# Kernel tuning notes

Hardware: AMD Instinct MI355X
Metric: run time of the kernel (lower is better)

The kernel has to match this reference:

```python
import jax, jax.numpy as jnp
import numpy as np

B, N, C = 8, 196, 512
NC, H = 10, 8
HD = C // H
SCALE = HD ** -0.5


def setup_inputs() -> dict:
    key = jax.random.key(0)
    ks = jax.random.split(key, 8)
    s = 1.0 / np.sqrt(C)
    return {
        "x": jax.random.normal(ks[0], (B, N, C), jnp.float32),
        "anchors": jax.random.normal(ks[1], (NC, N, C), jnp.float32),
        "weights": jax.random.uniform(ks[2], (B, H, NC), jnp.float32),
        "Wqk": jax.random.normal(ks[3], (C, C), jnp.float32) * s,
        "Wqk2": jax.random.normal(ks[4], (C, C), jnp.float32) * s,
        "Wv": jax.random.normal(ks[5], (C, C), jnp.float32) * s,
        "Wproj": jax.random.normal(ks[6], (C, C), jnp.float32) * s,
        "bproj": jax.random.normal(ks[7], (C,), jnp.float32) * 0.01,
    }


def _heads(t):
    # (..., N, C) -> (..., H, N, HD)
    shp = t.shape[:-2]
    return t.reshape(shp + (t.shape[-2], H, HD)).swapaxes(-3, -2)


def reference(x, anchors, weights, Wqk, Wqk2, Wv, Wproj, bproj):
    v = _heads(x @ Wv)                      # (B, H, N, HD)
    q = _heads(x @ Wqk)[:, None]            # (B, 1, H, N, HD)
    k = _heads(anchors @ Wqk)[None]         # (1, NC, H, N, HD)
    q2 = _heads(x @ Wqk2)[:, None]          # (B, 1, H, N, HD)
    k2 = _heads(anchors @ Wqk2)[None]       # (1, NC, H, N, HD)

    # ReLU-clipped double attention, both (B, NC, H, N, N)
    left_attn = jnp.maximum(-(q @ k.swapaxes(-2, -1)) * SCALE, 0.0)
    right_attn = jnp.maximum((k2 @ q2.swapaxes(-2, -1)) * SCALE, 0.0)

    attn = left_attn @ right_attn           # (B, NC, H, N, N)
    # per-head class-weighted combine: (B,H,NC) x (B,NC,H,N,N) -> (B,H,N,N)
    tmp = jnp.einsum('bhc,bchnm->bhnm', weights, attn)
    out = tmp @ v                           # (B, H, N, HD)
    # NOTE: original torch code reshapes (B,H,N,HD)->(B,N,C) WITHOUT a
    # transpose back; we replicate that exact flatten order.
    out = out.reshape(B, N, C)
    out = out @ Wproj + bproj
    return (out, left_attn)
```

## Files before the change

kernel.cpp:

```cpp
#include <hip/hip_runtime.h>

#define OFF_XB     0u
#define OFF_AB     1605632u
#define OFF_WQKT   3612672u
#define OFF_WQK2T  4136960u
#define OFF_WVT    4661248u
#define OFF_WPROJT 5185536u
#define OFF_XQ     5709824u
#define OFF_XQ2    7315456u
#define OFF_XV     8921088u
#define OFF_AQ     10526720u
#define OFF_AQ2    12533760u
#define OFF_RVT    14540800u
#define OFF_OUT1   35512320u
#define OFF_P      37117952u

typedef __attribute__((ext_vector_type(8))) short bf16x8;
typedef __attribute__((ext_vector_type(4))) float f32x4;
#define MFMA(a, b, c) __builtin_amdgcn_mfma_f32_16x16x32_bf16((a), (b), (c), 0, 0, 0)

__device__ __forceinline__ unsigned short f2bf(float x) {
  unsigned u = __builtin_bit_cast(unsigned, x);
  u += 0x7fffu + ((u >> 16) & 1u);
  return (unsigned short)(u >> 16);
}
__device__ __forceinline__ float bf2f(unsigned short s) {
  return __builtin_bit_cast(float, ((unsigned)s) << 16);
}

__device__ __forceinline__ void gl_lds16(const void* g, void* l) {
  __builtin_amdgcn_global_load_lds(
      (const __attribute__((address_space(1))) unsigned int*)g,
      (__attribute__((address_space(3))) unsigned int*)l, 16, 0, 0);
}

__device__ __forceinline__ void stage64(const unsigned short* g0, int stride,
                                        unsigned short (*T)[72], int tid, int nrows) {
  int wv = tid >> 6;
  char* base = (char*)&T[0][0];
#pragma unroll
  for (int i = 0; i < 2; i++) {
    int k = i * 256 + tid;
    int r = k / 9, c = k - r * 9;
    if (r < nrows)
      gl_lds16(g0 + (size_t)r * stride + (c << 3), base + (((i << 2) + wv) << 10));
  }
  if (tid < 64) {
    int k = 512 + tid;
    int r = k / 9, c = k - r * 9;
    if (r < nrows)
      gl_lds16(g0 + (size_t)r * stride + (c << 3), base + 8192);
  }
}

__device__ __forceinline__ void load_bf16_tile(unsigned short T[64][72], const unsigned short* __restrict__ g,
                                               int row0, int nrows, int col0, int tid) {
  int r = tid >> 2;
  int c0 = (tid & 3) << 4;
  uint4 a = make_uint4(0, 0, 0, 0), b = make_uint4(0, 0, 0, 0);
  if (r < nrows) {
    const unsigned short* p = g + (size_t)(row0 + r) * 512 + col0 + c0;
    a = *(const uint4*)p;
    b = *(const uint4*)(p + 8);
  }
  *(uint4*)&T[r][c0] = a;
  *(uint4*)&T[r][c0 + 8] = b;
}

__device__ __forceinline__ void load_bf16_tile_T(unsigned short T[64][72], const unsigned short* __restrict__ g,
                                                 int row0, int nrows, int col0, int tid) {
#pragma unroll
  for (int rep = 0; rep < 2; rep++) {
    int j = (tid >> 3) + (rep << 5);
    int d0 = (tid & 7) << 3;
    uint4 a = make_uint4(0, 0, 0, 0);
    if (j < nrows) a = *(const uint4*)(g + (size_t)(row0 + j) * 512 + col0 + d0);
    unsigned short s[8];
    *(uint4*)s = a;
#pragma unroll
    for (int u = 0; u < 8; u++) T[d0 + u][j] = s[u];
  }
}

__global__ __launch_bounds__(256) void pre_kernel(const float* __restrict__ x, const float* __restrict__ anchors,
                                                  const float* __restrict__ Wqk, const float* __restrict__ Wqk2,
                                                  const float* __restrict__ Wv, const float* __restrict__ Wproj,
                                                  char* __restrict__ ws) {
  int tid = threadIdx.x;
  if (blockIdx.x < 1764) {
    int base = blockIdx.x * 1024 + (tid << 2);
    float4 f = (base < 802816) ? *(const float4*)(x + base)
                               : *(const float4*)(anchors + (base - 802816));
    unsigned short s[4] = {f2bf(f.x), f2bf(f.y), f2bf(f.z), f2bf(f.w)};
    *(uint2*)((unsigned short*)(ws + OFF_XB) + base) = *(uint2*)s;
    return;
  }
  __shared__ unsigned short Ls[64][72];
  int idx = blockIdx.x - 1764;
  int wsel = idx >> 6, t = idx & 63;
  int k0 = (t >> 3) << 6, n0 = (t & 7) << 6;
  const float* W;
  unsigned short* WT;
  switch (wsel) {
    case 0:  W = Wqk;   WT = (unsigned short*)(ws + OFF_WQKT);   break;
    case 1:  W = Wqk2;  WT = (unsigned short*)(ws + OFF_WQK2T);  break;
    case 2:  W = Wv;    WT = (unsigned short*)(ws + OFF_WVT);    break;
    default: W = Wproj; WT = (unsigned short*)(ws + OFF_WPROJT); break;
  }
  {
    int r = tid >> 2, seg = (tid & 3) << 4;
    const float* p = W + (size_t)(k0 + r) * 512 + n0 + seg;
    float4 f0 = *(const float4*)p, f1 = *(const float4*)(p + 4);
    float4 f2 = *(const float4*)(p + 8), f3 = *(const float4*)(p + 12);
    unsigned short s[16] = {f2bf(f0.x), f2bf(f0.y), f2bf(f0.z), f2bf(f0.w),
                            f2bf(f1.x), f2bf(f1.y), f2bf(f1.z), f2bf(f1.w),
                            f2bf(f2.x), f2bf(f2.y), f2bf(f2.z), f2bf(f2.w),
                            f2bf(f3.x), f2bf(f3.y), f2bf(f3.z), f2bf(f3.w)};
    *(uint4*)&Ls[r][seg] = *(uint4*)s;
    *(uint4*)&Ls[r][seg + 8] = *(uint4*)(s + 8);
  }
  __syncthreads();
  {
    int r = tid >> 2, seg = (tid & 3) << 4;
    unsigned short s[16];
#pragma unroll
    for (int u = 0; u < 16; u++) s[u] = Ls[seg + u][r];
    unsigned short* dst = WT + (size_t)(n0 + r) * 512 + k0 + seg;
    *(uint4*)dst = *(uint4*)s;
    *(uint4*)(dst + 8) = *(uint4*)(s + 8);
  }
}

template <bool STORE_BF16>
__device__ __forceinline__ void gemm_bf16_body(const unsigned short* __restrict__ A,
                                               const unsigned short* __restrict__ WT,
                                               const float* __restrict__ bias, void* __restrict__ outp,
                                               int M, int row_blk, int col_blk) {
  __shared__ unsigned short As[64][72];
  __shared__ unsigned short Ws[64][72];
  int row0 = row_blk << 6;
  if (row0 >= M) return;
  int col0 = col_blk << 6;
  int tid = threadIdx.x;
  int w = tid >> 6, lm = tid & 15, lq = (tid >> 4) & 3;
  f32x4 acc[4] = {};
  for (int k0 = 0; k0 < 512; k0 += 64) {
    __syncthreads();
    stage64(A + (size_t)row0 * 512 + k0, 512, As, tid, 64);
    stage64(WT + (size_t)col0 * 512 + k0, 512, Ws, tid, 64);
    __syncthreads();
#pragma unroll
    for (int kk = 0; kk < 2; kk++) {
      bf16x8 bf = *(const bf16x8*)&Ws[(w << 4) + lm][(kk << 5) + (lq << 3)];
#pragma unroll
      for (int mi = 0; mi < 4; mi++) {
        bf16x8 af = *(const bf16x8*)&As[(mi << 4) + lm][(kk << 5) + (lq << 3)];
        acc[mi] = MFMA(af, bf, acc[mi]);
      }
    }
  }
  int ncol = col0 + (w << 4) + lm;
  float bv = bias ? bias[ncol] : 0.f;
#pragma unroll
  for (int mi = 0; mi < 4; mi++)
#pragma unroll
    for (int r2 = 0; r2 < 4; r2++) {
      int row = row0 + (mi << 4) + (lq << 2) + r2;
      if (row < M) {
        if (STORE_BF16)
          ((unsigned short*)outp)[(size_t)row * 512 + ncol] = f2bf(acc[mi][r2]);
        else
          ((float*)outp)[(size_t)row * 512 + ncol] = acc[mi][r2] + bv;
      }
    }
}

__global__ __launch_bounds__(256) void proj5(char* __restrict__ ws) {
  const unsigned short* xb = (const unsigned short*)(ws + OFF_XB);
  const unsigned short* ab = (const unsigned short*)(ws + OFF_AB);
  const unsigned short* A; const unsigned short* WT; unsigned short* O; int M;
  switch (blockIdx.z) {
    case 0:  A = xb; WT = (unsigned short*)(ws + OFF_WQKT);  O = (unsigned short*)(ws + OFF_XQ);  M = 1568; break;
    case 1:  A = xb; WT = (unsigned short*)(ws + OFF_WQK2T); O = (unsigned short*)(ws + OFF_XQ2); M = 1568; break;
    case 2:  A = xb; WT = (unsigned short*)(ws + OFF_WVT);   O = (unsigned short*)(ws + OFF_XV);  M = 1568; break;
    case 3:  A = ab; WT = (unsigned short*)(ws + OFF_WQKT);  O = (unsigned short*)(ws + OFF_AQ);  M = 1960; break;
    default: A = ab; WT = (unsigned short*)(ws + OFF_WQK2T); O = (unsigned short*)(ws + OFF_AQ2); M = 1960; break;
  }
  gemm_bf16_body<true>(A, WT, nullptr, O, M, blockIdx.x, blockIdx.y);
}

__global__ __launch_bounds__(256) void final_gemm(const unsigned short* __restrict__ out1,
                                                  const unsigned short* __restrict__ WT,
                                                  const float* __restrict__ bias, float* __restrict__ out) {
  gemm_bf16_body<false>(out1, WT, bias, out, 1568, blockIdx.x, blockIdx.y);
}

__global__ __launch_bounds__(256) void rv_mfma(char* __restrict__ ws) {
  const unsigned short* xq2 = (const unsigned short*)(ws + OFF_XQ2);
  const unsigned short* aq2 = (const unsigned short*)(ws + OFF_AQ2);
  const unsigned short* xv  = (const unsigned short*)(ws + OFF_XV);
  unsigned short* rvt       = (unsigned short*)(ws + OFF_RVT);
  __shared__ unsigned short Ks[64][72];
  __shared__ unsigned short Qs[64][72];
  __shared__ unsigned short Vt[64][72];
  __shared__ unsigned short Ss[64][72];
  int i0 = blockIdx.x << 6;
  int bch = blockIdx.y;
  int h = bch & 7, bc = bch >> 3;
  int c = bc % 10, b = bc / 10;
  int tid = threadIdx.x;
  int w = tid >> 6, lm = tid & 15, lq = (tid >> 4) & 3;
  int ni = min(64, 196 - i0);

  load_bf16_tile(Ks, aq2, c * 196 + i0, ni, h << 6, tid);
  __syncthreads();
  bf16x8 kf[4][2];
#pragma unroll
  for (int mi = 0; mi < 4; mi++)
#pragma unroll
    for (int kk = 0; kk < 2; kk++)
      kf[mi][kk] = *(const bf16x8*)&Ks[(mi << 4) + lm][(kk << 5) + (lq << 3)];

  f32x4 acc[4] = {};
  for (int jt = 0; jt < 4; jt++) {
    int j0 = jt << 6;
    int nj = min(64, 196 - j0);
    __syncthreads();
    stage64(xq2 + (size_t)(b * 196 + j0) * 512 + (h << 6), 512, Qs, tid, 64);
    load_bf16_tile_T(Vt, xv, b * 196 + j0, nj, h << 6, tid);
    __syncthreads();
    f32x4 s[4] = {};
#pragma unroll
    for (int kk = 0; kk < 2; kk++) {
      bf16x8 bf = *(const bf16x8*)&Qs[(w << 4) + lm][(kk << 5) + (lq << 3)];
#pragma unroll
      for (int mi = 0; mi < 4; mi++) s[mi] = MFMA(kf[mi][kk], bf, s[mi]);
    }
#pragma unroll
    for (int mi = 0; mi < 4; mi++)
#pragma unroll
      for (int r = 0; r < 4; r++)
        Ss[(mi << 4) + (lq << 2) + r][(w << 4) + lm] = f2bf(fmaxf(0.125f * s[mi][r], 0.f));
    __syncthreads();
#pragma unroll
    for (int kk = 0; kk < 2; kk++) {
      bf16x8 bf = *(const bf16x8*)&Vt[(w << 4) + lm][(kk << 5) + (lq << 3)];
#pragma unroll
      for (int mi = 0; mi < 4; mi++) {
        bf16x8 af = *(const bf16x8*)&Ss[(mi << 4) + lm][(kk << 5) + (lq << 3)];
        acc[mi] = MFMA(af, bf, acc[mi]);
      }
    }
  }
  __syncthreads();
#pragma unroll
  for (int mi = 0; mi < 4; mi++)
#pragma unroll
    for (int r = 0; r < 4; r++)
      Ss[(w << 4) + lm][(mi << 4) + (lq << 2) + r] = f2bf(acc[mi][r]);
  __syncthreads();
  {
    int dd = tid >> 2, seg = (tid & 3) << 4;
    unsigned short* dst = rvt + ((size_t)(bch * 4 + blockIdx.x) * 64 + dd) * 64 + seg;
    *(uint4*)dst = *(uint4*)&Ss[dd][seg];
    *(uint4*)(dst + 8) = *(uint4*)&Ss[dd][seg + 8];
  }
}

__global__ __launch_bounds__(256) void attn_mfma(char* __restrict__ ws, float* __restrict__ left,
                                                 unsigned short* __restrict__ P) {
  const unsigned short* xq  = (const unsigned short*)(ws + OFF_XQ);
  const unsigned short* aq  = (const unsigned short*)(ws + OFF_AQ);
  const unsigned short* rvt = (const unsigned short*)(ws + OFF_RVT);
  __shared__ unsigned short Qs[64][72];
  __shared__ unsigned short Ks[64][72];
  __shared__ unsigned short Rt[64][72];
  __shared__ unsigned short Ss[64][72];
  int i0 = blockIdx.x << 6;
  int bh = blockIdx.y;
  int c = blockIdx.z;
  int b = bh >> 3, h = bh & 7;
  int bch = (b * 10 + c) * 8 + h;
  int tid = threadIdx.x;
  int w = tid >> 6, lm = tid & 15, lq = (tid >> 4) & 3;

  stage64(xq + (size_t)(b * 196 + i0) * 512 + (h << 6), 512, Qs, tid, 64);
  bf16x8 qf[4][2];
  f32x4 acc[4] = {};
  size_t lbase = (size_t)bch * (196 * 196);
#pragma unroll
  for (int t = 0; t < 4; t++) {
    int jt = (t == 0) ? 3 : t - 1;
    int j0 = jt << 6;
    int nj = (jt == 3) ? 4 : 64;
    __syncthreads();
    if (t == 0) {
      uint4 z = make_uint4(0, 0, 0, 0);
      for (int k = tid; k < 540; k += 256)
        *(uint4*)((char*)&Ks[0][0] + 576 + k * 16) = z;
    }
    stage64(aq + (size_t)(c * 196 + j0) * 512 + (h << 6), 512, Ks, tid, nj);
    stage64(rvt + (size_t)(bch * 4 + jt) * 4096, 64, Rt, tid, 64);
    __syncthreads();
    if (t == 0) {
#pragma unroll
      for (int mi = 0; mi < 4; mi++)
#pragma unroll
        for (int kk = 0; kk < 2; kk++)
          qf[mi][kk] = *(const bf16x8*)&Qs[(mi << 4) + lm][(kk << 5) + (lq << 3)];
    }
    f32x4 s[4] = {};
#pragma unroll
    for (int kk = 0; kk < 2; kk++) {
      bf16x8 bf = *(const bf16x8*)&Ks[(w << 4) + lm][(kk << 5) + (lq << 3)];
#pragma unroll
      for (int mi = 0; mi < 4; mi++) s[mi] = MFMA(qf[mi][kk], bf, s[mi]);
    }
#pragma unroll
    for (int mi = 0; mi < 4; mi++)
#pragma unroll
      for (int r = 0; r < 4; r++) {
        float v = fmaxf(-0.125f * s[mi][r], 0.f);
        int il = (mi << 4) + (lq << 2) + r;
        int jl = (w << 4) + lm;
        Ss[il][jl] = f2bf(v);
        if (i0 + il < 196 && j0 + jl < 196)
          left[lbase + (size_t)(i0 + il) * 196 + (j0 + jl)] = v;
      }
    __syncthreads();
#pragma unroll
    for (int kk = 0; kk < 2; kk++) {
      bf16x8 bf = *(const bf16x8*)&Rt[(w << 4) + lm][(kk << 5) + (lq << 3)];
#pragma unroll
      for (int mi = 0; mi < 4; mi++) {
        bf16x8 af = *(const bf16x8*)&Ss[(mi << 4) + lm][(kk << 5) + (lq << 3)];
        acc[mi] = MFMA(af, bf, acc[mi]);
      }
    }
  }
  __syncthreads();
#pragma unroll
  for (int mi = 0; mi < 4; mi++)
#pragma unroll
    for (int r = 0; r < 4; r++)
      Ss[(mi << 4) + (lq << 2) + r][(w << 4) + lm] = f2bf(acc[mi][r]);
  __syncthreads();
  {
    int row = tid >> 2, seg = (tid & 3) << 4;
    if (i0 + row < 196) {
      unsigned short* dst = P + ((size_t)(bh * 10 + c) * 196 + i0 + row) * 64 + seg;
      *(uint4*)dst = *(uint4*)&Ss[row][seg];
      *(uint4*)(dst + 8) = *(uint4*)&Ss[row][seg + 8];
    }
  }
}

__global__ __launch_bounds__(256) void reduce_out1(const unsigned short* __restrict__ P,
                                                   const float* __restrict__ weights,
                                                   unsigned short* __restrict__ out1) {
  int t = blockIdx.x * 256 + threadIdx.x;
  int base = t << 2;
  int bh = base / 12544;
  int rem = base - bh * 12544;
  const float* wrow = weights + bh * 10;
  float a0 = 0.f, a1 = 0.f, a2 = 0.f, a3 = 0.f;
#pragma unroll
  for (int c = 0; c < 10; c++) {
    float wc = wrow[c];
    const unsigned short* p = P + ((size_t)(bh * 10 + c)) * 12544 + rem;
    ushort4 u = *(const ushort4*)p;
    a0 = fmaf(wc, bf2f(u.x), a0);
    a1 = fmaf(wc, bf2f(u.y), a1);
    a2 = fmaf(wc, bf2f(u.z), a2);
    a3 = fmaf(wc, bf2f(u.w), a3);
  }
  unsigned short s[4] = {f2bf(a0), f2bf(a1), f2bf(a2), f2bf(a3)};
  *(uint2*)&out1[base] = *(uint2*)s;
}

extern "C" void kernel_launch(void* const* d_in, const int* in_sizes, int n_in,
                              void* d_out, int out_size, void* d_ws, size_t ws_size,
                              hipStream_t stream) {
  (void)in_sizes; (void)n_in; (void)out_size; (void)ws_size;
  const float* x       = (const float*)d_in[0];
  const float* anchors = (const float*)d_in[1];
  const float* weights = (const float*)d_in[2];
  const float* Wqk     = (const float*)d_in[3];
  const float* Wqk2    = (const float*)d_in[4];
  const float* Wv      = (const float*)d_in[5];
  const float* Wproj   = (const float*)d_in[6];
  const float* bproj   = (const float*)d_in[7];
  char* ws = (char*)d_ws;
  float* out  = (float*)d_out;
  float* left = out + 802816;

  dim3 blk(256);
  pre_kernel<<<dim3(2020), blk, 0, stream>>>(x, anchors, Wqk, Wqk2, Wv, Wproj, ws);
  proj5<<<dim3(31, 8, 5), blk, 0, stream>>>(ws);
  rv_mfma<<<dim3(4, 640), blk, 0, stream>>>(ws);
  attn_mfma<<<dim3(4, 64, 10), blk, 0, stream>>>(ws, left, (unsigned short*)(ws + OFF_P));
  reduce_out1<<<dim3(784), blk, 0, stream>>>((const unsigned short*)(ws + OFF_P), weights,
                                             (unsigned short*)(ws + OFF_OUT1));
  final_gemm<<<dim3(25, 8), blk, 0, stream>>>((const unsigned short*)(ws + OFF_OUT1),
                                              (const unsigned short*)(ws + OFF_WPROJT), bproj, out);
}
```

Before: 231.2 us.

## Fuse right-attention-times-V and left-attention kernels into one per-(b,c,h) block

Merges the rv_mfma and attn_mfma kernels into one kernel with one block per (batch, class, head). The right_attn@V product is kept in registers (rf) and is no longer written to and re-read from the workspace, and one kernel launch is removed. In exchange the grid shrinks from 2560 blocks per kernel to 640, each doing four times more serial work, which may reduce parallelism and latency hiding on a GPU with many CUs.

```diff
diff --git a/kernel.cpp b/kernel.cpp
--- a/kernel.cpp
+++ b/kernel.cpp
@@ -195,162 +195,150 @@
   gemm_bf16_body<false>(out1, WT, bias, out, 1568, blockIdx.x, blockIdx.y);
 }
 
-__global__ __launch_bounds__(256) void rv_mfma(char* __restrict__ ws) {
+__global__ __launch_bounds__(256) void rv_attn(char* __restrict__ ws, float* __restrict__ left,
+                                               unsigned short* __restrict__ P) {
   const unsigned short* xq2 = (const unsigned short*)(ws + OFF_XQ2);
   const unsigned short* aq2 = (const unsigned short*)(ws + OFF_AQ2);
   const unsigned short* xv  = (const unsigned short*)(ws + OFF_XV);
-  unsigned short* rvt       = (unsigned short*)(ws + OFF_RVT);
+  const unsigned short* xq  = (const unsigned short*)(ws + OFF_XQ);
+  const unsigned short* aq  = (const unsigned short*)(ws + OFF_AQ);
   __shared__ unsigned short Ks[64][72];
   __shared__ unsigned short Qs[64][72];
   __shared__ unsigned short Vt[64][72];
   __shared__ unsigned short Ss[64][72];
-  int i0 = blockIdx.x << 6;
-  int bch = blockIdx.y;
+  int bch = blockIdx.x;
   int h = bch & 7, bc = bch >> 3;
   int c = bc % 10, b = bc / 10;
+  int bh = (b << 3) + h;
   int tid = threadIdx.x;
   int w = tid >> 6, lm = tid & 15, lq = (tid >> 4) & 3;
-  int ni = min(64, 196 - i0);
-
-  load_bf16_tile(Ks, aq2, c * 196 + i0, ni, h << 6, tid);
-  __syncthreads();
-  bf16x8 kf[4][2];
-#pragma unroll
-  for (int mi = 0; mi < 4; mi++)
+
+  bf16x8 rf[4][2];
+
+#pragma unroll
+  for (int it = 0; it < 4; it++) {
+    int i0 = it << 6;
+    int ni = (it == 3) ? 4 : 64;
+    load_bf16_tile(Ks, aq2, c * 196 + i0, ni, h << 6, tid);
+    __syncthreads();
+    bf16x8 kf[4][2];
+#pragma unroll
+    for (int mi = 0; mi < 4; mi++)
+#pragma unroll
+      for (int kk = 0; kk < 2; kk++)
+        kf[mi][kk] = *(const bf16x8*)&Ks[(mi << 4) + lm][(kk << 5) + (lq << 3)];
+
+    f32x4 acc[4] = {};
+    for (int jt = 0; jt < 4; jt++) {
+      int j0 = jt << 6;
+      int nj = min(64, 196 - j0);
+      __syncthreads();
+      stage64(xq2 + (size_t)(b * 196 + j0) * 512 + (h << 6), 512, Qs, tid, 64);
+      load_bf16_tile_T(Vt, xv, b * 196 + j0, nj, h << 6, tid);
+      __syncthreads();
+      f32x4 s[4] = {};
+#pragma unroll
+      for (int kk = 0; kk < 2; kk++) {
+        bf16x8 bf = *(const bf16x8*)&Qs[(w << 4) + lm][(kk << 5) + (lq << 3)];
+#pragma unroll
+        for (int mi = 0; mi < 4; mi++) s[mi] = MFMA(kf[mi][kk], bf, s[mi]);
+      }
+#pragma unroll
+      for (int mi = 0; mi < 4; mi++)
+#pragma unroll
+        for (int r = 0; r < 4; r++)
+          Ss[(mi << 4) + (lq << 2) + r][(w << 4) + lm] = f2bf(fmaxf(0.125f * s[mi][r], 0.f));
+      __syncthreads();
+#pragma unroll
+      for (int kk = 0; kk < 2; kk++) {
+        bf16x8 bf = *(const bf16x8*)&Vt[(w << 4) + lm][(kk << 5) + (lq << 3)];
+#pragma unroll
+        for (int mi = 0; mi < 4; mi++) {
+          bf16x8 af = *(const bf16x8*)&Ss[(mi << 4) + lm][(kk << 5) + (lq << 3)];
+          acc[mi] = MFMA(af, bf, acc[mi]);
+        }
+      }
+    }
+    __syncthreads();
+#pragma unroll
+    for (int mi = 0; mi < 4; mi++)
+#pragma unroll
+      for (int r = 0; r < 4; r++)
+        Ss[(w << 4) + lm][(mi << 4) + (lq << 2) + r] = f2bf(acc[mi][r]);
+    __syncthreads();
 #pragma unroll
     for (int kk = 0; kk < 2; kk++)
-      kf[mi][kk] = *(const bf16x8*)&Ks[(mi << 4) + lm][(kk << 5) + (lq << 3)];
-
-  f32x4 acc[4] = {};
-  for (int jt = 0; jt < 4; jt++) {
-    int j0 = jt << 6;
-    int nj = min(64, 196 - j0);
-    __syncthreads();
-    stage64(xq2 + (size_t)(b * 196 + j0) * 512 + (h << 6), 512, Qs, tid, 64);
-    load_bf16_tile_T(Vt, xv, b * 196 + j0, nj, h << 6, tid);
-    __syncthreads();
-    f32x4 s[4] = {};
-#pragma unroll
-    for (int kk = 0; kk < 2; kk++) {
-      bf16x8 bf = *(const bf16x8*)&Qs[(w << 4) + lm][(kk << 5) + (lq << 3)];
-#pragma unroll
-      for (int mi = 0; mi < 4; mi++) s[mi] = MFMA(kf[mi][kk], bf, s[mi]);
-    }
+      rf[it][kk] = *(const bf16x8*)&Ss[(w << 4) + lm][(kk << 5) + (lq << 3)];
+  }
+
+  size_t lbase = (size_t)bch * (196 * 196);
+  for (int it = 0; it < 4; it++) {
+    int i0 = it << 6;
+    stage64(xq + (size_t)(b * 196 + i0) * 512 + (h << 6), 512, Qs, tid, 64);
+    bf16x8 qf[4][2];
+    f32x4 acc[4] = {};
+#pragma unroll
+    for (int t = 0; t < 4; t++) {
+      int jt = (t == 0) ? 3 : t - 1;
+      int j0 = jt << 6;
+      int nj = (jt == 3) ? 4 : 64;
+      __syncthreads();
+      if (t == 0) {
+        uint4 z = make_uint4(0, 0, 0, 0);
+        for (int k = tid; k < 540; k += 256)
+          *(uint4*)((char*)&Ks[0][0] + 576 + k * 16) = z;
+      }
+      stage64(aq + (size_t)(c * 196 + j0) * 512 + (h << 6), 512, Ks, tid, nj);
+      __syncthreads();
+      if (t == 0) {
+#pragma unroll
+        for (int mi = 0; mi < 4; mi++)
+#pragma unroll
+          for (int kk = 0; kk < 2; kk++)
+            qf[mi][kk] = *(const bf16x8*)&Qs[(mi << 4) + lm][(kk << 5) + (lq << 3)];
+      }
+      f32x4 s[4] = {};
+#pragma unroll
+      for (int kk = 0; kk < 2; kk++) {
+        bf16x8 bf = *(const bf16x8*)&Ks[(w << 4) + lm][(kk << 5) + (lq << 3)];
+#pragma unroll
+        for (int mi = 0; mi < 4; mi++) s[mi] = MFMA(qf[mi][kk], bf, s[mi]);
+      }
+#pragma unroll
+      for (int mi = 0; mi < 4; mi++)
+#pragma unroll
+        for (int r = 0; r < 4; r++) {
+          float v = fmaxf(-0.125f * s[mi][r], 0.f);
+          int il = (mi << 4) + (lq << 2) + r;
+          int jl = (w << 4) + lm;
+          Ss[il][jl] = f2bf(v);
+          if (i0 + il < 196 && j0 + jl < 196)
+            left[lbase + (size_t)(i0 + il) * 196 + (j0 + jl)] = v;
+        }
+      __syncthreads();
+#pragma unroll
+      for (int kk = 0; kk < 2; kk++) {
+#pragma unroll
+        for (int mi = 0; mi < 4; mi++) {
+          bf16x8 af = *(const bf16x8*)&Ss[(mi << 4) + lm][(kk << 5) + (lq << 3)];
+          acc[mi] = MFMA(af, rf[jt][kk], acc[mi]);
+        }
+      }
+    }
+    __syncthreads();
 #pragma unroll
     for (int mi = 0; mi < 4; mi++)
 #pragma unroll
       for (int r = 0; r < 4; r++)
-        Ss[(mi << 4) + (lq << 2) + r][(w << 4) + lm] = f2bf(fmaxf(0.125f * s[mi][r], 0.f));
-    __syncthreads();
-#pragma unroll
-    for (int kk = 0; kk < 2; kk++) {
-      bf16x8 bf = *(const bf16x8*)&Vt[(w << 4) + lm][(kk << 5) + (lq << 3)];
-#pragma unroll
-      for (int mi = 0; mi < 4; mi++) {
-        bf16x8 af = *(const bf16x8*)&Ss[(mi << 4) + lm][(kk << 5) + (lq << 3)];
-        acc[mi] = MFMA(af, bf, acc[mi]);
-      }
-    }
-  }
-  __syncthreads();
-#pragma unroll
-  for (int mi = 0; mi < 4; mi++)
-#pragma unroll
-    for (int r = 0; r < 4; r++)
-      Ss[(w << 4) + lm][(mi << 4) + (lq << 2) + r] = f2bf(acc[mi][r]);
-  __syncthreads();
-  {
-    int dd = tid >> 2, seg = (tid & 3) << 4;
-    unsigned short* dst = rvt + ((size_t)(bch * 4 + blockIdx.x) * 64 + dd) * 64 + seg;
-    *(uint4*)dst = *(uint4*)&Ss[dd][seg];
-    *(uint4*)(dst + 8) = *(uint4*)&Ss[dd][seg + 8];
-  }
-}
-
-__global__ __launch_bounds__(256) void attn_mfma(char* __restrict__ ws, float* __restrict__ left,
-                                                 unsigned short* __restrict__ P) {
-  const unsigned short* xq  = (const unsigned short*)(ws + OFF_XQ);
-  const unsigned short* aq  = (const unsigned short*)(ws + OFF_AQ);
-  const unsigned short* rvt = (const unsigned short*)(ws + OFF_RVT);
-  __shared__ unsigned short Qs[64][72];
-  __shared__ unsigned short Ks[64][72];
-  __shared__ unsigned short Rt[64][72];
-  __shared__ unsigned short Ss[64][72];
-  int i0 = blockIdx.x << 6;
-  int bh = blockIdx.y;
-  int c = blockIdx.z;
-  int b = bh >> 3, h = bh & 7;
-  int bch = (b * 10 + c) * 8 + h;
-  int tid = threadIdx.x;
-  int w = tid >> 6, lm = tid & 15, lq = (tid >> 4) & 3;
-
-  stage64(xq + (size_t)(b * 196 + i0) * 512 + (h << 6), 512, Qs, tid, 64);
-  bf16x8 qf[4][2];
-  f32x4 acc[4] = {};
-  size_t lbase = (size_t)bch * (196 * 196);
-#pragma unroll
-  for (int t = 0; t < 4; t++) {
-    int jt = (t == 0) ? 3 : t - 1;
-    int j0 = jt << 6;
-    int nj = (jt == 3) ? 4 : 64;
-    __syncthreads();
-    if (t == 0) {
-      uint4 z = make_uint4(0, 0, 0, 0);
-      for (int k = tid; k < 540; k += 256)
-        *(uint4*)((char*)&Ks[0][0] + 576 + k * 16) = z;
-    }
-    stage64(aq + (size_t)(c * 196 + j0) * 512 + (h << 6), 512, Ks, tid, nj);
-    stage64(rvt + (size_t)(bch * 4 + jt) * 4096, 64, Rt, tid, 64);
-    __syncthreads();
-    if (t == 0) {
-#pragma unroll
-      for (int mi = 0; mi < 4; mi++)
-#pragma unroll
-        for (int kk = 0; kk < 2; kk++)
-          qf[mi][kk] = *(const bf16x8*)&Qs[(mi << 4) + lm][(kk << 5) + (lq << 3)];
-    }
-    f32x4 s[4] = {};
-#pragma unroll
-    for (int kk = 0; kk < 2; kk++) {
-      bf16x8 bf = *(const bf16x8*)&Ks[(w << 4) + lm][(kk << 5) + (lq << 3)];
-#pragma unroll
-      for (int mi = 0; mi < 4; mi++) s[mi] = MFMA(qf[mi][kk], bf, s[mi]);
-    }
-#pragma unroll
-    for (int mi = 0; mi < 4; mi++)
-#pragma unroll
-      for (int r = 0; r < 4; r++) {
-        float v = fmaxf(-0.125f * s[mi][r], 0.f);
-        int il = (mi << 4) + (lq << 2) + r;
-        int jl = (w << 4) + lm;
-        Ss[il][jl] = f2bf(v);
-        if (i0 + il < 196 && j0 + jl < 196)
-          left[lbase + (size_t)(i0 + il) * 196 + (j0 + jl)] = v;
-      }
-    __syncthreads();
-#pragma unroll
-    for (int kk = 0; kk < 2; kk++) {
-      bf16x8 bf = *(const bf16x8*)&Rt[(w << 4) + lm][(kk << 5) + (lq << 3)];
-#pragma unroll
-      for (int mi = 0; mi < 4; mi++) {
-        bf16x8 af = *(const bf16x8*)&Ss[(mi << 4) + lm][(kk << 5) + (lq << 3)];
-        acc[mi] = MFMA(af, bf, acc[mi]);
-      }
-    }
-  }
-  __syncthreads();
-#pragma unroll
-  for (int mi = 0; mi < 4; mi++)
-#pragma unroll
-    for (int r = 0; r < 4; r++)
-      Ss[(mi << 4) + (lq << 2) + r][(w << 4) + lm] = f2bf(acc[mi][r]);
-  __syncthreads();
-  {
-    int row = tid >> 2, seg = (tid & 3) << 4;
-    if (i0 + row < 196) {
-      unsigned short* dst = P + ((size_t)(bh * 10 + c) * 196 + i0 + row) * 64 + seg;
-      *(uint4*)dst = *(uint4*)&Ss[row][seg];
-      *(uint4*)(dst + 8) = *(uint4*)&Ss[row][seg + 8];
+        Ss[(mi << 4) + (lq << 2) + r][(w << 4) + lm] = f2bf(acc[mi][r]);
+    __syncthreads();
+    {
+      int row = tid >> 2, seg = (tid & 3) << 4;
+      if (i0 + row < 196) {
+        unsigned short* dst = P + ((size_t)(bh * 10 + c) * 196 + i0 + row) * 64 + seg;
+        *(uint4*)dst = *(uint4*)&Ss[row][seg];
+        *(uint4*)(dst + 8) = *(uint4*)&Ss[row][seg + 8];
+      }
     }
   }
 }
@@ -397,8 +385,7 @@
   dim3 blk(256);
   pre_kernel<<<dim3(2020), blk, 0, stream>>>(x, anchors, Wqk, Wqk2, Wv, Wproj, ws);
   proj5<<<dim3(31, 8, 5), blk, 0, stream>>>(ws);
-  rv_mfma<<<dim3(4, 640), blk, 0, stream>>>(ws);
-  attn_mfma<<<dim3(4, 64, 10), blk, 0, stream>>>(ws, left, (unsigned short*)(ws + OFF_P));
+  rv_attn<<<dim3(640), blk, 0, stream>>>(ws, left, (unsigned short*)(ws + OFF_P));
   reduce_out1<<<dim3(784), blk, 0, stream>>>((const unsigned short*)(ws + OFF_P), weights,
                                              (unsigned short*)(ws + OFF_OUT1));
   final_gemm<<<dim3(25, 8), blk, 0, stream>>>((const unsigned short*)(ws + OFF_OUT1),
```

Result: slower. 240.0 us (+3.8%).

## Swap MFMA operand roles, prefetch next tiles, vectorize left_attn stores

Applied to the files above, without the earlier changes.

The rv and attn kernels now swap the MFMA operand roles, so each lane holds a full row segment and writes S and the left_attn output as packed uint2 and float4 stores instead of scalar strided ones. Loading of the next K/Q and V tiles is moved to overlap with the second MFMA phase, which removes one barrier per iteration and acts as a software prefetch. The rvt operand is now read straight from global memory into registers, so the Rt shared buffer goes away and LDS use drops. The risk is correctness of the reordered staging and barriers, plus higher register pressure from the prefetch.

```diff
diff --git a/kernel.cpp b/kernel.cpp
--- a/kernel.cpp
+++ b/kernel.cpp
@@ -67,19 +67,23 @@
   *(uint4*)&T[r][c0 + 8] = b;
 }
 
-__device__ __forceinline__ void load_bf16_tile_T(unsigned short T[64][72], const unsigned short* __restrict__ g,
-                                                 int row0, int nrows, int col0, int tid) {
-#pragma unroll
-  for (int rep = 0; rep < 2; rep++) {
-    int j = (tid >> 3) + (rep << 5);
-    int d0 = (tid & 7) << 3;
-    uint4 a = make_uint4(0, 0, 0, 0);
-    if (j < nrows) a = *(const uint4*)(g + (size_t)(row0 + j) * 512 + col0 + d0);
-    unsigned short s[8];
-    *(uint4*)s = a;
-#pragma unroll
-    for (int u = 0; u < 8; u++) T[d0 + u][j] = s[u];
-  }
+__device__ __forceinline__ void vload_T(uint4* va, uint4* vb, const unsigned short* __restrict__ g,
+                                        int row0, int nrows, int col0, int tid) {
+  int j0 = tid >> 3, d0 = (tid & 7) << 3;
+  *va = make_uint4(0, 0, 0, 0);
+  *vb = make_uint4(0, 0, 0, 0);
+  if (j0 < nrows) *va = *(const uint4*)(g + (size_t)(row0 + j0) * 512 + col0 + d0);
+  if (j0 + 32 < nrows) *vb = *(const uint4*)(g + (size_t)(row0 + j0 + 32) * 512 + col0 + d0);
+}
+__device__ __forceinline__ void vwrite_T(unsigned short T[64][72], uint4 va, uint4 vb, int tid) {
+  int j0 = tid >> 3, d0 = (tid & 7) << 3;
+  unsigned short s[8];
+  *(uint4*)s = va;
+#pragma unroll
+  for (int u = 0; u < 8; u++) T[d0 + u][j0] = s[u];
+  *(uint4*)s = vb;
+#pragma unroll
+  for (int u = 0; u < 8; u++) T[d0 + u][j0 + 32] = s[u];
 }
 
 __global__ __launch_bounds__(256) void pre_kernel(const float* __restrict__ x, const float* __restrict__ anchors,
@@ -95,7 +99,7 @@
     *(uint2*)((unsigned short*)(ws + OFF_XB) + base) = *(uint2*)s;
     return;
   }
-  __shared__ unsigned short Ls[64][72];
+  __shared__ __align__(16) unsigned short Ls[64][72];
   int idx = blockIdx.x - 1764;
   int wsel = idx >> 6, t = idx & 63;
   int k0 = (t >> 3) << 6, n0 = (t & 7) << 6;
@@ -136,8 +140,8 @@
                                                const unsigned short* __restrict__ WT,
                                                const float* __restrict__ bias, void* __restrict__ outp,
                                                int M, int row_blk, int col_blk) {
-  __shared__ unsigned short As[64][72];
-  __shared__ unsigned short Ws[64][72];
+  __shared__ __align__(16) unsigned short As[64][72];
+  __shared__ __align__(16) unsigned short Ws[64][72];
   int row0 = row_blk << 6;
   if (row0 >= M) return;
   int col0 = col_blk << 6;
@@ -200,10 +204,10 @@
   const unsigned short* aq2 = (const unsigned short*)(ws + OFF_AQ2);
   const unsigned short* xv  = (const unsigned short*)(ws + OFF_XV);
   unsigned short* rvt       = (unsigned short*)(ws + OFF_RVT);
-  __shared__ unsigned short Ks[64][72];
-  __shared__ unsigned short Qs[64][72];
-  __shared__ unsigned short Vt[64][72];
-  __shared__ unsigned short Ss[64][72];
+  __shared__ __align__(16) unsigned short Ks[64][72];
+  __shared__ __align__(16) unsigned short Qs[64][72];
+  __shared__ __align__(16) unsigned short Vt[64][72];
+  __shared__ __align__(16) unsigned short Ss[64][72];
   int i0 = blockIdx.x << 6;
   int bch = blockIdx.y;
   int h = bch & 7, bc = bch >> 3;
@@ -213,35 +217,39 @@
   int ni = min(64, 196 - i0);
 
   load_bf16_tile(Ks, aq2, c * 196 + i0, ni, h << 6, tid);
-  __syncthreads();
-  bf16x8 kf[4][2];
-#pragma unroll
-  for (int mi = 0; mi < 4; mi++)
-#pragma unroll
-    for (int kk = 0; kk < 2; kk++)
-      kf[mi][kk] = *(const bf16x8*)&Ks[(mi << 4) + lm][(kk << 5) + (lq << 3)];
-
+  stage64(xq2 + (size_t)(b * 196) * 512 + (h << 6), 512, Qs, tid, 64);
+  uint4 va, vb;
+  vload_T(&va, &vb, xv, b * 196, 64, h << 6, tid);
+
+  bf16x8 kb[2];
   f32x4 acc[4] = {};
+#pragma unroll
   for (int jt = 0; jt < 4; jt++) {
     int j0 = jt << 6;
-    int nj = min(64, 196 - j0);
-    __syncthreads();
-    stage64(xq2 + (size_t)(b * 196 + j0) * 512 + (h << 6), 512, Qs, tid, 64);
-    load_bf16_tile_T(Vt, xv, b * 196 + j0, nj, h << 6, tid);
-    __syncthreads();
+    __syncthreads();
+    if (jt == 0) {
+#pragma unroll
+      for (int kk = 0; kk < 2; kk++)
+        kb[kk] = *(const bf16x8*)&Ks[(w << 4) + lm][(kk << 5) + (lq << 3)];
+    }
+    vwrite_T(Vt, va, vb, tid);
     f32x4 s[4] = {};
 #pragma unroll
-    for (int kk = 0; kk < 2; kk++) {
-      bf16x8 bf = *(const bf16x8*)&Qs[(w << 4) + lm][(kk << 5) + (lq << 3)];
-#pragma unroll
-      for (int mi = 0; mi < 4; mi++) s[mi] = MFMA(kf[mi][kk], bf, s[mi]);
-    }
-#pragma unroll
-    for (int mi = 0; mi < 4; mi++)
-#pragma unroll
-      for (int r = 0; r < 4; r++)
-        Ss[(mi << 4) + (lq << 2) + r][(w << 4) + lm] = f2bf(fmaxf(0.125f * s[mi][r], 0.f));
-    __syncthreads();
+    for (int kk = 0; kk < 2; kk++)
+#pragma unroll
+      for (int mj = 0; mj < 4; mj++) {
+        bf16x8 af = *(const bf16x8*)&Qs[(mj << 4) + lm][(kk << 5) + (lq << 3)];
+        s[mj] = MFMA(af, kb[kk], s[mj]);
+      }
+#pragma unroll
+    for (int mj = 0; mj < 4; mj++) {
+      unsigned short u[4] = {f2bf(fmaxf(0.125f * s[mj][0], 0.f)), f2bf(fmaxf(0.125f * s[mj][1], 0.f)),
+                             f2bf(fmaxf(0.125f * s[mj][2], 0.f)), f2bf(fmaxf(0.125f * s[mj][3], 0.f))};
+      *(uint2*)&Ss[(w << 4) + lm][(mj << 4) + (lq << 2)] = *(uint2*)u;
+    }
+    if (jt < 3) vload_T(&va, &vb, xv, b * 196 + j0 + 64, min(64, 196 - j0 - 64), h << 6, tid);
+    __syncthreads();
+    if (jt < 3) stage64(xq2 + (size_t)(b * 196 + j0 + 64) * 512 + (h << 6), 512, Qs, tid, 64);
 #pragma unroll
     for (int kk = 0; kk < 2; kk++) {
       bf16x8 bf = *(const bf16x8*)&Vt[(w << 4) + lm][(kk << 5) + (lq << 3)];
@@ -254,10 +262,10 @@
   }
   __syncthreads();
 #pragma unroll
-  for (int mi = 0; mi < 4; mi++)
-#pragma unroll
-    for (int r = 0; r < 4; r++)
-      Ss[(w << 4) + lm][(mi << 4) + (lq << 2) + r] = f2bf(acc[mi][r]);
+  for (int mi = 0; mi < 4; mi++) {
+    unsigned short u[4] = {f2bf(acc[mi][0]), f2bf(acc[mi][1]), f2bf(acc[mi][2]), f2bf(acc[mi][3])};
+    *(uint2*)&Ss[(w << 4) + lm][(mi << 4) + (lq << 2)] = *(uint2*)u;
+  }
   __syncthreads();
   {
     int dd = tid >> 2, seg = (tid & 3) << 4;
@@ -272,10 +280,9 @@
   const unsigned short* xq  = (const unsigned short*)(ws + OFF_XQ);
   const unsigned short* aq  = (const unsigned short*)(ws + OFF_AQ);
   const unsigned short* rvt = (const unsigned short*)(ws + OFF_RVT);
-  __shared__ unsigned short Qs[64][72];
-  __shared__ unsigned short Ks[64][72];
-  __shared__ unsigned short Rt[64][72];
-  __shared__ unsigned short Ss[64][72];
+  __shared__ __align__(16) unsigned short Qs[64][72];
+  __shared__ __align__(16) unsigned short Ks[64][72];
+  __shared__ __align__(16) unsigned short Ss[64][72];
   int i0 = blockIdx.x << 6;
   int bh = blockIdx.y;
   int c = blockIdx.z;
@@ -285,52 +292,57 @@
   int w = tid >> 6, lm = tid & 15, lq = (tid >> 4) & 3;
 
   stage64(xq + (size_t)(b * 196 + i0) * 512 + (h << 6), 512, Qs, tid, 64);
-  bf16x8 qf[4][2];
+  {
+    uint4 z = make_uint4(0, 0, 0, 0);
+    for (int k = tid; k < 540; k += 256)
+      *(uint4*)((char*)&Ks[0][0] + 576 + k * 16) = z;
+  }
+  stage64(aq + (size_t)(c * 196 + 192) * 512 + (h << 6), 512, Ks, tid, 4);
+
+  bf16x8 qb[2];
   f32x4 acc[4] = {};
   size_t lbase = (size_t)bch * (196 * 196);
+  int iglob = i0 + (w << 4) + lm;
 #pragma unroll
   for (int t = 0; t < 4; t++) {
     int jt = (t == 0) ? 3 : t - 1;
     int j0 = jt << 6;
-    int nj = (jt == 3) ? 4 : 64;
-    __syncthreads();
+    __syncthreads();
+    const unsigned short* rp = rvt + (size_t)(bch * 4 + jt) * 4096 + (((w << 4) + lm) << 6) + (lq << 3);
+    bf16x8 rvb0 = *(const bf16x8*)rp;
+    bf16x8 rvb1 = *(const bf16x8*)(rp + 32);
     if (t == 0) {
-      uint4 z = make_uint4(0, 0, 0, 0);
-      for (int k = tid; k < 540; k += 256)
-        *(uint4*)((char*)&Ks[0][0] + 576 + k * 16) = z;
-    }
-    stage64(aq + (size_t)(c * 196 + j0) * 512 + (h << 6), 512, Ks, tid, nj);
-    stage64(rvt + (size_t)(bch * 4 + jt) * 4096, 64, Rt, tid, 64);
-    __syncthreads();
-    if (t == 0) {
-#pragma unroll
-      for (int mi = 0; mi < 4; mi++)
-#pragma unroll
-        for (int kk = 0; kk < 2; kk++)
-          qf[mi][kk] = *(const bf16x8*)&Qs[(mi << 4) + lm][(kk << 5) + (lq << 3)];
+#pragma unroll
+      for (int kk = 0; kk < 2; kk++)
+        qb[kk] = *(const bf16x8*)&Qs[(w << 4) + lm][(kk << 5) + (lq << 3)];
     }
     f32x4 s[4] = {};
 #pragma unroll
+    for (int kk = 0; kk < 2; kk++)
+#pragma unroll
+      for (int mj = 0; mj < 4; mj++) {
+        bf16x8 af = *(const bf16x8*)&Ks[(mj << 4) + lm][(kk << 5) + (lq << 3)];
+        s[mj] = MFMA(af, qb[kk], s[mj]);
+      }
+#pragma unroll
+    for (int mj = 0; mj < 4; mj++) {
+      float4 lv;
+      lv.x = fmaxf(-0.125f * s[mj][0], 0.f);
+      lv.y = fmaxf(-0.125f * s[mj][1], 0.f);
+      lv.z = fmaxf(-0.125f * s[mj][2], 0.f);
+      lv.w = fmaxf(-0.125f * s[mj][3], 0.f);
+      int jloc = (mj << 4) + (lq << 2);
+      if (iglob < 196 && j0 + jloc < 196)
+        *(float4*)&left[lbase + (size_t)iglob * 196 + j0 + jloc] = lv;
+      unsigned short u[4] = {f2bf(lv.x), f2bf(lv.y), f2bf(lv.z), f2bf(lv.w)};
+      *(uint2*)&Ss[(w << 4) + lm][jloc] = *(uint2*)u;
+    }
+    __syncthreads();
+    if (t < 3)
+      stage64(aq + (size_t)(c * 196 + (t << 6)) * 512 + (h << 6), 512, Ks, tid, 64);
+#pragma unroll
     for (int kk = 0; kk < 2; kk++) {
-      bf16x8 bf = *(const bf16x8*)&Ks[(w << 4) + lm][(kk << 5) + (lq << 3)];
-#pragma unroll
-      for (int mi = 0; mi < 4; mi++) s[mi] = MFMA(qf[mi][kk], bf, s[mi]);
-    }
-#pragma unroll
-    for (int mi = 0; mi < 4; mi++)
-#pragma unroll
-      for (int r = 0; r < 4; r++) {
-        float v = fmaxf(-0.125f * s[mi][r], 0.f);
-        int il = (mi << 4) + (lq << 2) + r;
-        int jl = (w << 4) + lm;
-        Ss[il][jl] = f2bf(v);
-        if (i0 + il < 196 && j0 + jl < 196)
-          left[lbase + (size_t)(i0 + il) * 196 + (j0 + jl)] = v;
-      }
-    __syncthreads();
-#pragma unroll
-    for (int kk = 0; kk < 2; kk++) {
-      bf16x8 bf = *(const bf16x8*)&Rt[(w << 4) + lm][(kk << 5) + (lq << 3)];
+      bf16x8 bf = (kk == 0) ? rvb0 : rvb1;
 #pragma unroll
       for (int mi = 0; mi < 4; mi++) {
         bf16x8 af = *(const bf16x8*)&Ss[(mi << 4) + lm][(kk << 5) + (lq << 3)];
```

After: 232.4 us. Within noise of the previous version (+0.5%).
